# Kernel tuning notes

Hardware: AMD Instinct MI355X
Metric: run time of the kernel (lower is better)

## Reference

```python
import jax, jax.numpy as jnp
import numpy as np

N = 262144          # batch size
C = 100             # num_classes
R0, R1 = 0.95, 1.0  # recall_range
LAM = 0.5           # lambda_pauc
LS = 0.1            # label_smoothing
MAX_PAUC = R1 - R0


def setup_inputs() -> dict:
    key = jax.random.key(0)
    k1, k2 = jax.random.split(key)
    predictions = jax.random.normal(k1, (N, C), dtype=jnp.float32)
    targets = jax.random.randint(k2, (N,), 0, C)
    weight = jnp.ones((C,), dtype=jnp.float32)
    return {"predictions": predictions, "targets": targets, "weight": weight}


def _roc_curves(scores, labels):
    """Vectorized per-class ROC. scores, labels: [C, N].
    Replaces the O(N^2) per-threshold loop with sort + cumsum (tie-correct:
    tp at threshold s_j counts ALL samples with score >= s_j)."""
    order = jnp.argsort(-scores, axis=1)                      # descending
    ss = jnp.take_along_axis(scores, order, axis=1)           # [C, N]
    sl = jnp.take_along_axis(labels, order, axis=1)           # [C, N]
    cpos = jnp.cumsum(sl, axis=1)                             # cumulative positives
    # last index within each tie-group of equal scores
    neg = -ss  # ascending
    idx = jax.vmap(lambda a: jnp.searchsorted(a, a, side='right'))(neg) - 1
    tp = jnp.take_along_axis(cpos, idx, axis=1)
    cnt = (idx + 1).astype(scores.dtype)
    fp = cnt - tp
    P = cpos[:, -1:]                       # total positives per class
    Nn = scores.shape[1] - P               # total negatives per class
    tpr = jnp.where(P > 0, tp / jnp.maximum(P, 1.0), 0.0)
    fpr = jnp.where(Nn > 0, fp / jnp.maximum(Nn, 1.0), 0.0)
    return fpr, tpr


def reference(predictions, targets, weight):
    probs = jax.nn.softmax(predictions, axis=1)               # [N, C]
    onehot = jnp.eye(C, dtype=predictions.dtype)[targets]     # [N, C]
    onehot_s = (1.0 - LS) * onehot + LS / C

    # per-class binary labels (smoothed true-class value > 0.5)
    labels = (onehot_s > 0.5).astype(predictions.dtype).T     # [C, N]
    scores = probs.T                                          # [C, N]

    fpr, tpr = _roc_curves(scores, labels)
    mask = (tpr >= R0) & (tpr <= R1)
    y = jnp.maximum(tpr - R0, 0.0)
    # tpr is monotone non-decreasing, so the recall mask is contiguous and
    # trapz over the masked subset == sum over adjacent pairs both in mask.
    pm = (mask[:, :-1] & mask[:, 1:]).astype(predictions.dtype)
    pauc = jnp.sum(0.5 * (y[:, :-1] + y[:, 1:]) * (fpr[:, 1:] - fpr[:, :-1]) * pm, axis=1)  # [C]

    avg_p_auc = jnp.sum(pauc * weight) / (jnp.sum(weight) * MAX_PAUC)
    # torch computes TP/FP via .item(): the pAUC path carries no gradient
    avg_p_auc = jax.lax.stop_gradient(jnp.clip(avg_p_auc, 0.0, 1.0))

    log_probs = jax.nn.log_softmax(predictions, axis=1)
    ce_loss = -jnp.mean(jnp.sum(onehot_s * log_probs * weight, axis=1))
    pauc_loss = 1.0 - avg_p_auc ** 2
    return (1.0 - LAM) * ce_loss + LAM * pauc_loss
```

## Files before the change

### kernel.cpp

```cpp
#include <hip/hip_runtime.h>
#include <math.h>

#define WAVE 64
constexpr int   CC      = 100;
constexpr int   MAXM    = 160;
constexpr int   BUCKET  = 4096;
constexpr int   USTRIDE = 161;
constexpr int   LCAP    = 4096;
constexpr float LSMOOTH = 0.1f;
constexpr int   TILE    = 64;

__global__ __launch_bounds__(256) void k1_tile(
    const float* __restrict__ pred, const int* __restrict__ targets,
    const float* __restrict__ weight, float* __restrict__ L_out,
    float* __restrict__ pos_out, float* __restrict__ ce_partial, int N)
{
    __shared__ float tile[TILE * CC];
    __shared__ int   ttgt[TILE];
    __shared__ float tL[TILE], tpos[TILE];
    __shared__ float cered[4];
    const int tid = threadIdx.x;
    const int r0  = blockIdx.x * TILE;

    const float4* src = (const float4*)(pred + (size_t)r0 * CC);
    #pragma unroll
    for (int t = tid; t < TILE * (CC / 4); t += 256)
        *((float4*)&tile[t * 4]) = src[t];
    if (tid < TILE) ttgt[tid] = targets[r0 + tid];
    __syncthreads();

    const int x = tid & 15;
    const int G = tid >> 4;
    float w[7];
    #pragma unroll
    for (int j = 0; j < 7; ++j) {
        int c = x + 16 * j;
        w[j] = (c < CC) ? weight[c] : 0.0f;
    }
    float Wl = 0.0f;
    #pragma unroll
    for (int j = 0; j < 7; ++j) Wl += w[j];
    #pragma unroll
    for (int off = 1; off < 16; off <<= 1) Wl += __shfl_xor(Wl, off, 16);

    float ce_acc = 0.0f;
    #pragma unroll
    for (int rr = 0; rr < 4; ++rr) {
        const int r = G * 4 + rr;
        const float* rp = tile + r * CC;
        float v[7];
        #pragma unroll
        for (int j = 0; j < 7; ++j) {
            int c = x + 16 * j;
            v[j] = (c < CC) ? rp[c] : -INFINITY;
        }
        float vmax = v[0];
        #pragma unroll
        for (int j = 1; j < 7; ++j) vmax = fmaxf(vmax, v[j]);
        #pragma unroll
        for (int off = 1; off < 16; off <<= 1) vmax = fmaxf(vmax, __shfl_xor(vmax, off, 16));
        float z = 0.0f, ws = 0.0f;
        #pragma unroll
        for (int j = 0; j < 7; ++j) {
            int c = x + 16 * j;
            if (c < CC) { z += __expf(v[j] - vmax); ws += w[j] * v[j]; }
        }
        #pragma unroll
        for (int off = 1; off < 16; off <<= 1) {
            z  += __shfl_xor(z,  off, 16);
            ws += __shfl_xor(ws, off, 16);
        }
        float L = vmax + __logf(z);
        if (x == 0) {
            int t = ttgt[r];
            float pt = rp[t];
            tL[r] = L; tpos[r] = pt - L;
            ce_acc += -((1.0f - LSMOOTH) * weight[t] * (pt - L)
                        + (LSMOOTH / CC) * (ws - Wl * L));
        }
    }
    #pragma unroll
    for (int off = 32; off; off >>= 1) ce_acc += __shfl_xor(ce_acc, off, WAVE);
    if ((tid & 63) == 0) cered[tid >> 6] = ce_acc;
    __syncthreads();
    if (tid < TILE) {
        L_out[r0 + tid]   = tL[tid];
        pos_out[r0 + tid] = tpos[tid];
    }
    if (tid == 0)
        ce_partial[blockIdx.x] = cered[0] + cered[1] + cered[2] + cered[3];
}

__global__ __launch_bounds__(256) void k1b_scatter(
    const int* __restrict__ targets, const float* __restrict__ pos,
    int* __restrict__ cls_cnt, float* __restrict__ bucket, int N)
{
    __shared__ int hist[CC];
    __shared__ int base[CC];
    __shared__ int loc[CC];
    const int tid = threadIdx.x;
    const int rowsPerBlock = N / gridDim.x;
    const int r0 = blockIdx.x * rowsPerBlock;
    const int r1 = r0 + rowsPerBlock;
    for (int c = tid; c < CC; c += blockDim.x) { hist[c] = 0; loc[c] = 0; }
    __syncthreads();
    for (int r = r0 + tid; r < r1; r += blockDim.x)
        atomicAdd(&hist[targets[r]], 1);
    __syncthreads();
    for (int c = tid; c < CC; c += blockDim.x)
        base[c] = (hist[c] > 0) ? atomicAdd(&cls_cnt[c], hist[c]) : 0;
    __syncthreads();
    for (int r = r0 + tid; r < r1; r += blockDim.x) {
        int c = targets[r];
        int idx = base[c] + atomicAdd(&loc[c], 1);
        if (idx < BUCKET) bucket[(size_t)c * BUCKET + idx] = pos[r];
    }
}

__global__ __launch_bounds__(256) void k2_select(
    const float* __restrict__ bucket, const int* __restrict__ cls_cnt,
    float* __restrict__ u, int* __restrict__ m_arr, int* __restrict__ P_arr,
    float* __restrict__ wm_arr)
{
    __shared__ unsigned int keys[BUCKET];
    __shared__ unsigned int hist[256];
    __shared__ unsigned int scan[256];
    __shared__ unsigned int sel[256];
    __shared__ unsigned int s_prefix;
    __shared__ int s_rank;
    __shared__ int cnt_lt;
    const int c   = blockIdx.x;
    const int tid = threadIdx.x;
    const int P = min(cls_cnt[c], BUCKET);
    double Kd = 0.95 * (double)P;
    int kf = (int)floor(Kd);
    int m = P - kf;
    if (m > MAXM) m = MAXM;
    if (m < 0) m = 0;
    if (tid == 0) {
        m_arr[c] = m; P_arr[c] = P;
        wm_arr[c] = (float)((double)(kf + 1) - Kd);
        s_prefix = 0; s_rank = m - 1; cnt_lt = 0;
    }
    for (int i = tid; i < P; i += 256) {
        unsigned int b = __float_as_uint(bucket[(size_t)c * BUCKET + i]);
        keys[i] = (b & 0x80000000u) ? ~b : (b | 0x80000000u);
    }
    __syncthreads();
    if (m == 0) return;

    for (int shift = 24; shift >= 0; shift -= 8) {
        hist[tid] = 0;
        __syncthreads();
        unsigned int pref = s_prefix;
        for (int i = tid; i < P; i += 256) {
            unsigned int k = keys[i];
            bool match = (shift == 24) || ((k >> (shift + 8)) == pref);
            if (match) atomicAdd(&hist[(k >> shift) & 255u], 1u);
        }
        __syncthreads();
        scan[tid] = hist[tid];
        __syncthreads();
        for (int off = 1; off < 256; off <<= 1) {
            unsigned int add = (tid >= off) ? scan[tid - off] : 0u;
            __syncthreads();
            scan[tid] += add;
            __syncthreads();
        }
        int r = s_rank;
        unsigned int inc = scan[tid];
        unsigned int exc = inc - hist[tid];
        __syncthreads();
        if ((unsigned int)r >= exc && (unsigned int)r < inc) {
            s_rank   = r - (int)exc;
            s_prefix = (pref << 8) | (unsigned int)tid;
        }
        __syncthreads();
    }
    const unsigned int kth = s_prefix;

    for (int i = tid; i < P; i += 256) {
        unsigned int k = keys[i];
        if (k < kth) {
            int pslot = atomicAdd(&cnt_lt, 1);
            sel[pslot] = k;
        }
    }
    __syncthreads();
    const int nlt = cnt_lt;
    for (int j = nlt + tid; j < 256; j += 256) sel[j] = (j < m) ? kth : 0xFFFFFFFFu;
    __syncthreads();
    for (int kk = 2; kk <= 256; kk <<= 1) {
        for (int j = kk >> 1; j > 0; j >>= 1) {
            int i = tid, ixj = tid ^ j;
            if (ixj > i) {
                unsigned int a = sel[i], b = sel[ixj];
                bool up = ((i & kk) == 0);
                if ((a > b) == up) { sel[i] = b; sel[ixj] = a; }
            }
            __syncthreads();
        }
    }
    if (tid < m) {
        unsigned int k = sel[tid];
        unsigned int b = (k & 0x80000000u) ? (k & 0x7fffffffu) : ~k;
        u[c * MAXM + tid] = __uint_as_float(b);
    }
}

__device__ __forceinline__ int ubound(const float* uc, int m, float key, int maxidx) {
    int l = 0;
    #pragma unroll
    for (int s = 128; s; s >>= 1) {
        int p = l + s - 1;
        float val = uc[p < maxidx ? p : maxidx];
        l += ((p < m) && (val <= key)) ? s : 0;
    }
    return l;
}

__global__ __launch_bounds__(256) void k3a_stream(
    const float4* __restrict__ pred4, const float* __restrict__ L,
    const float* __restrict__ u, const int* __restrict__ m_arr,
    uint2* __restrict__ list, int* __restrict__ list_cnt, int list_cap,
    int* __restrict__ g_cnt, int* __restrict__ g_sum, int total4)
{
    __shared__ float umax_s[CC];
    __shared__ uint2 buf[LCAP];
    __shared__ int lcnt;
    __shared__ int gbase;
    const int tid = threadIdx.x;
    if (tid < CC) {
        int m = m_arr[tid];
        umax_s[tid] = (m > 0) ? u[tid * MAXM + m - 1] : -INFINITY;
    }
    if (tid == 0) lcnt = 0;
    __syncthreads();

    const int stride = gridDim.x * blockDim.x;
    int i = blockIdx.x * blockDim.x + tid;
    int j = i % 25;
    int n = i / 25;
    const int dj = stride % 25, dn = stride / 25;
    while (i < total4) {
        float4 v = pred4[i];
        float Ln = L[n];
        float4 um = *((const float4*)&umax_s[j * 4]);
        float s0 = v.x - Ln, s1 = v.y - Ln, s2 = v.z - Ln, s3 = v.w - Ln;
        #pragma unroll
        for (int q = 0; q < 4; ++q) {
            float sc = (q == 0) ? s0 : (q == 1) ? s1 : (q == 2) ? s2 : s3;
            float mx = (q == 0) ? um.x : (q == 1) ? um.y : (q == 2) ? um.z : um.w;
            if (sc < mx) {
                int c = j * 4 + q;
                int idx = atomicAdd(&lcnt, 1);
                if (idx < LCAP) {
                    buf[idx] = make_uint2((unsigned int)c, __float_as_uint(sc));
                } else {
                    int m = m_arr[c];
                    int l = ubound(u + c * MAXM, m, sc, MAXM - 1);
                    atomicAdd(&g_cnt[c], 1);
                    atomicAdd(&g_sum[c], m - 1 - l);
                }
            }
        }
        i += stride; j += dj; n += dn;
        if (j >= 25) { j -= 25; n += 1; }
    }
    __syncthreads();
    int cnt = min(lcnt, LCAP);
    if (tid == 0) gbase = atomicAdd(list_cnt, cnt);
    __syncthreads();
    const int base0 = gbase;
    for (int k = tid; k < cnt; k += 256) {
        int gi = base0 + k;
        if (gi < list_cap) {
            list[gi] = buf[k];
        } else {
            uint2 e = buf[k];
            int c = (int)e.x; float sc = __uint_as_float(e.y);
            int m = m_arr[c];
            int l = ubound(u + c * MAXM, m, sc, MAXM - 1);
            atomicAdd(&g_cnt[c], 1);
            atomicAdd(&g_sum[c], m - 1 - l);
        }
    }
}

__global__ __launch_bounds__(256) void k3b_rank(
    const uint2* __restrict__ list, const int* __restrict__ list_cnt, int list_cap,
    const float* __restrict__ u, const int* __restrict__ m_arr,
    int* __restrict__ g_cnt, int* __restrict__ g_sum)
{
    __shared__ float us[CC * USTRIDE];
    __shared__ int sm[CC];
    __shared__ int lcnt[CC], lsum[CC];
    const int tid = threadIdx.x;
    for (int c = tid; c < CC; c += 256) { sm[c] = m_arr[c]; lcnt[c] = 0; lsum[c] = 0; }
    for (int t = tid; t < CC * MAXM; t += 256) {
        int c = t / MAXM, k = t - c * MAXM;
        us[c * USTRIDE + k] = u[t];
    }
    __syncthreads();
    const int n = min(*list_cnt, list_cap);
    const int stride = gridDim.x * blockDim.x;
    for (int idx = blockIdx.x * blockDim.x + tid; idx < n; idx += stride) {
        uint2 e = list[idx];
        int c = (int)e.x;
        float key = __uint_as_float(e.y);
        int m = sm[c];
        int l = ubound(us + c * USTRIDE, m, key, USTRIDE - 1);
        atomicAdd(&lcnt[c], 1);
        atomicAdd(&lsum[c], m - 1 - l);
    }
    __syncthreads();
    for (int c = tid; c < CC; c += 256) {
        if (lcnt[c]) { atomicAdd(&g_cnt[c], lcnt[c]); atomicAdd(&g_sum[c], lsum[c]); }
    }
}

__global__ __launch_bounds__(256) void k4_final(
    const float* __restrict__ ce_partial, int nPartial,
    const float* __restrict__ weight, const int* __restrict__ P_arr,
    const int* __restrict__ m_arr, const float* __restrict__ wm_arr,
    const int* __restrict__ g_cnt, const int* __restrict__ g_sum,
    float* __restrict__ out, int N)
{
    __shared__ double r1[256], r2[256], r3[256];
    double ce = 0.0;
    for (int i = threadIdx.x; i < nPartial; i += blockDim.x) ce += (double)ce_partial[i];
    double p = 0.0, wsum = 0.0;
    for (int c = threadIdx.x; c < CC; c += blockDim.x) {
        int P = P_arr[c], m = m_arr[c];
        double wgt = (double)weight[c];
        long long Nn = (long long)N - P;
        if (P > 0 && Nn > 0 && m > 0) {
            double wm = (double)wm_arr[c];
            double S   = (double)g_sum[c] + wm * (double)g_cnt[c];
            double sub = 0.5 * (double)(m - 1) * (double)(m - 2) + wm * (double)(m - 1);
            double pc  = (S - sub) / ((double)Nn * (double)P);
            if (pc < 0.0) pc = 0.0;
            p += pc * wgt;
        }
        wsum += wgt;
    }
    r1[threadIdx.x] = ce; r2[threadIdx.x] = p; r3[threadIdx.x] = wsum;
    __syncthreads();
    for (int off = blockDim.x >> 1; off; off >>= 1) {
        if ((int)threadIdx.x < off) {
            r1[threadIdx.x] += r1[threadIdx.x + off];
            r2[threadIdx.x] += r2[threadIdx.x + off];
            r3[threadIdx.x] += r3[threadIdx.x + off];
        }
        __syncthreads();
    }
    if (threadIdx.x == 0) {
        double ce_loss = r1[0] / (double)N;
        double avg = r2[0] / (r3[0] * 0.05);
        avg = fmin(fmax(avg, 0.0), 1.0);
        out[0] = (float)(0.5 * ce_loss + 0.5 * (1.0 - avg * avg));
    }
}

extern "C" void kernel_launch(void* const* d_in, const int* in_sizes, int n_in,
                              void* d_out, int out_size, void* d_ws, size_t ws_size,
                              hipStream_t stream) {
    (void)n_in; (void)out_size;
    const float* pred    = (const float*)d_in[0];
    const int*   targets = (const int*)d_in[1];
    const float* weight  = (const float*)d_in[2];
    float* out = (float*)d_out;
    const int N = in_sizes[1];

    const int K1_BLOCKS = N / TILE;
    char* base = (char*)d_ws;
    size_t off = 0;
    auto take = [&](size_t bytes) { char* q = base + off; off += (bytes + 15) & ~(size_t)15; return q; };
    float* L_ws       = (float*)take((size_t)N * 4);
    float* pos_ws     = (float*)take((size_t)N * 4);
    float* ce_partial = (float*)take((size_t)K1_BLOCKS * 4);
    float* u          = (float*)take((size_t)CC * MAXM * 4);
    int*   m_arr      = (int*)take(CC * 4);
    int*   P_arr      = (int*)take(CC * 4);
    float* wm_arr     = (float*)take(CC * 4);
    int*   zero_blk   = (int*)take(304 * 4);
    int*   cls_cnt  = zero_blk;
    int*   g_cnt    = zero_blk + CC;
    int*   g_sum    = zero_blk + 2 * CC;
    int*   list_cnt = zero_blk + 3 * CC;
    float* bucket     = (float*)take((size_t)CC * BUCKET * 4);
    uint2* list       = (uint2*)(base + off);
    long long rem     = (long long)ws_size - (long long)off;
    int list_cap      = (rem > 0) ? (int)(rem / 8) : 0;

    hipMemsetAsync(zero_blk, 0, 304 * 4, stream);

    k1_tile<<<K1_BLOCKS, 256, 0, stream>>>(pred, targets, weight, L_ws, pos_ws,
                                           ce_partial, N);
    k1b_scatter<<<256, 256, 0, stream>>>(targets, pos_ws, cls_cnt, bucket, N);
    k2_select<<<CC, 256, 0, stream>>>(bucket, cls_cnt, u, m_arr, P_arr, wm_arr);
    const int total4 = (int)((size_t)N * CC / 4);
    k3a_stream<<<1024, 256, 0, stream>>>((const float4*)pred, L_ws, u, m_arr,
                                         list, list_cnt, list_cap, g_cnt, g_sum, total4);
    k3b_rank<<<512, 256, 0, stream>>>(list, list_cnt, list_cap, u, m_arr, g_cnt, g_sum);
    k4_final<<<1, 256, 0, stream>>>(ce_partial, K1_BLOCKS, weight, P_arr, m_arr, wm_arr,
                                    g_cnt, g_sum, out, N);
}
```

Before: 261.9 us.

## Fuse stream, rank and final reduction into one kernel with last-block finish

Merges the candidate-streaming, ranking and final-reduction kernels into a single kernel. Each block ranks its own shared-memory candidate buffer against u in global memory and aggregates per-class counts locally. The last block to finish, detected with an atomic counter, computes the final loss. The hipMemset is replaced by zeroing inside k1. This removes three launches, the global list round-trip and the memset, at the cost of ranking against u from global/L2 instead of an LDS copy.

```diff
diff --git a/kernel.cpp b/kernel.cpp
--- a/kernel.cpp
+++ b/kernel.cpp
@@ -5,15 +5,16 @@
 constexpr int   CC      = 100;
 constexpr int   MAXM    = 160;
 constexpr int   BUCKET  = 4096;
-constexpr int   USTRIDE = 161;
 constexpr int   LCAP    = 4096;
 constexpr float LSMOOTH = 0.1f;
 constexpr int   TILE    = 64;
+constexpr int   ZN      = 3 * CC + 8;
 
 __global__ __launch_bounds__(256) void k1_tile(
     const float* __restrict__ pred, const int* __restrict__ targets,
     const float* __restrict__ weight, float* __restrict__ L_out,
-    float* __restrict__ pos_out, float* __restrict__ ce_partial, int N)
+    float* __restrict__ pos_out, float* __restrict__ ce_partial,
+    int* __restrict__ zero_blk, int N)
 {
     __shared__ float tile[TILE * CC];
     __shared__ int   ttgt[TILE];
@@ -21,6 +22,9 @@
     __shared__ float cered[4];
     const int tid = threadIdx.x;
     const int r0  = blockIdx.x * TILE;
+
+    if (blockIdx.x == 0)
+        for (int i = tid; i < ZN; i += 256) zero_blk[i] = 0;
 
     const float4* src = (const float4*)(pred + (size_t)r0 * CC);
     #pragma unroll
@@ -219,22 +223,30 @@
     return l;
 }
 
-__global__ __launch_bounds__(256) void k3a_stream(
+__global__ __launch_bounds__(256) void k3_fused(
     const float4* __restrict__ pred4, const float* __restrict__ L,
     const float* __restrict__ u, const int* __restrict__ m_arr,
-    uint2* __restrict__ list, int* __restrict__ list_cnt, int list_cap,
-    int* __restrict__ g_cnt, int* __restrict__ g_sum, int total4)
+    int* __restrict__ g_cnt, int* __restrict__ g_sum, int* __restrict__ done,
+    const float* __restrict__ ce_partial, int nPartial,
+    const float* __restrict__ weight, const int* __restrict__ P_arr,
+    const float* __restrict__ wm_arr, float* __restrict__ out,
+    int N, int total4)
 {
     __shared__ float umax_s[CC];
+    __shared__ int   sm[CC];
+    __shared__ int   lcnt[CC], lsum[CC];
     __shared__ uint2 buf[LCAP];
-    __shared__ int lcnt;
-    __shared__ int gbase;
+    __shared__ int   lc;
+    __shared__ int   isLast;
+    __shared__ double r1[256], r2[256], r3[256];
     const int tid = threadIdx.x;
     if (tid < CC) {
         int m = m_arr[tid];
+        sm[tid] = m;
         umax_s[tid] = (m > 0) ? u[tid * MAXM + m - 1] : -INFINITY;
-    }
-    if (tid == 0) lcnt = 0;
+        lcnt[tid] = 0; lsum[tid] = 0;
+    }
+    if (tid == 0) lc = 0;
     __syncthreads();
 
     const int stride = gridDim.x * blockDim.x;
@@ -253,14 +265,14 @@
             float mx = (q == 0) ? um.x : (q == 1) ? um.y : (q == 2) ? um.z : um.w;
             if (sc < mx) {
                 int c = j * 4 + q;
-                int idx = atomicAdd(&lcnt, 1);
+                int idx = atomicAdd(&lc, 1);
                 if (idx < LCAP) {
                     buf[idx] = make_uint2((unsigned int)c, __float_as_uint(sc));
                 } else {
-                    int m = m_arr[c];
+                    int m = sm[c];
                     int l = ubound(u + c * MAXM, m, sc, MAXM - 1);
-                    atomicAdd(&g_cnt[c], 1);
-                    atomicAdd(&g_sum[c], m - 1 - l);
+                    atomicAdd(&lcnt[c], 1);
+                    atomicAdd(&lsum[c], m - 1 - l);
                 }
             }
         }
@@ -268,48 +280,14 @@
         if (j >= 25) { j -= 25; n += 1; }
     }
     __syncthreads();
-    int cnt = min(lcnt, LCAP);
-    if (tid == 0) gbase = atomicAdd(list_cnt, cnt);
-    __syncthreads();
-    const int base0 = gbase;
+
+    const int cnt = min(lc, LCAP);
     for (int k = tid; k < cnt; k += 256) {
-        int gi = base0 + k;
-        if (gi < list_cap) {
-            list[gi] = buf[k];
-        } else {
-            uint2 e = buf[k];
-            int c = (int)e.x; float sc = __uint_as_float(e.y);
-            int m = m_arr[c];
-            int l = ubound(u + c * MAXM, m, sc, MAXM - 1);
-            atomicAdd(&g_cnt[c], 1);
-            atomicAdd(&g_sum[c], m - 1 - l);
-        }
-    }
-}
-
-__global__ __launch_bounds__(256) void k3b_rank(
-    const uint2* __restrict__ list, const int* __restrict__ list_cnt, int list_cap,
-    const float* __restrict__ u, const int* __restrict__ m_arr,
-    int* __restrict__ g_cnt, int* __restrict__ g_sum)
-{
-    __shared__ float us[CC * USTRIDE];
-    __shared__ int sm[CC];
-    __shared__ int lcnt[CC], lsum[CC];
-    const int tid = threadIdx.x;
-    for (int c = tid; c < CC; c += 256) { sm[c] = m_arr[c]; lcnt[c] = 0; lsum[c] = 0; }
-    for (int t = tid; t < CC * MAXM; t += 256) {
-        int c = t / MAXM, k = t - c * MAXM;
-        us[c * USTRIDE + k] = u[t];
-    }
-    __syncthreads();
-    const int n = min(*list_cnt, list_cap);
-    const int stride = gridDim.x * blockDim.x;
-    for (int idx = blockIdx.x * blockDim.x + tid; idx < n; idx += stride) {
-        uint2 e = list[idx];
+        uint2 e = buf[k];
         int c = (int)e.x;
         float key = __uint_as_float(e.y);
         int m = sm[c];
-        int l = ubound(us + c * USTRIDE, m, key, USTRIDE - 1);
+        int l = ubound(u + c * MAXM, m, key, MAXM - 1);
         atomicAdd(&lcnt[c], 1);
         atomicAdd(&lsum[c], m - 1 - l);
     }
@@ -317,26 +295,27 @@
     for (int c = tid; c < CC; c += 256) {
         if (lcnt[c]) { atomicAdd(&g_cnt[c], lcnt[c]); atomicAdd(&g_sum[c], lsum[c]); }
     }
-}
-
-__global__ __launch_bounds__(256) void k4_final(
-    const float* __restrict__ ce_partial, int nPartial,
-    const float* __restrict__ weight, const int* __restrict__ P_arr,
-    const int* __restrict__ m_arr, const float* __restrict__ wm_arr,
-    const int* __restrict__ g_cnt, const int* __restrict__ g_sum,
-    float* __restrict__ out, int N)
-{
-    __shared__ double r1[256], r2[256], r3[256];
+
+    if (tid == 0) {
+        __threadfence();
+        int t = atomicAdd(done, 1);
+        isLast = (t == (int)gridDim.x - 1);
+    }
+    __syncthreads();
+    if (!isLast) return;
+    __threadfence();
+
     double ce = 0.0;
-    for (int i = threadIdx.x; i < nPartial; i += blockDim.x) ce += (double)ce_partial[i];
+    for (int k = tid; k < nPartial; k += 256) ce += (double)ce_partial[k];
     double p = 0.0, wsum = 0.0;
-    for (int c = threadIdx.x; c < CC; c += blockDim.x) {
-        int P = P_arr[c], m = m_arr[c];
+    for (int c = tid; c < CC; c += 256) {
+        int P = P_arr[c], m = sm[c];
         double wgt = (double)weight[c];
         long long Nn = (long long)N - P;
         if (P > 0 && Nn > 0 && m > 0) {
             double wm = (double)wm_arr[c];
-            double S   = (double)g_sum[c] + wm * (double)g_cnt[c];
+            double S   = (double)atomicAdd(&g_sum[c], 0)
+                       + wm * (double)atomicAdd(&g_cnt[c], 0);
             double sub = 0.5 * (double)(m - 1) * (double)(m - 2) + wm * (double)(m - 1);
             double pc  = (S - sub) / ((double)Nn * (double)P);
             if (pc < 0.0) pc = 0.0;
@@ -344,17 +323,17 @@
         }
         wsum += wgt;
     }
-    r1[threadIdx.x] = ce; r2[threadIdx.x] = p; r3[threadIdx.x] = wsum;
-    __syncthreads();
-    for (int off = blockDim.x >> 1; off; off >>= 1) {
-        if ((int)threadIdx.x < off) {
-            r1[threadIdx.x] += r1[threadIdx.x + off];
-            r2[threadIdx.x] += r2[threadIdx.x + off];
-            r3[threadIdx.x] += r3[threadIdx.x + off];
-        }
-        __syncthreads();
-    }
-    if (threadIdx.x == 0) {
+    r1[tid] = ce; r2[tid] = p; r3[tid] = wsum;
+    __syncthreads();
+    for (int off = 128; off; off >>= 1) {
+        if (tid < off) {
+            r1[tid] += r1[tid + off];
+            r2[tid] += r2[tid + off];
+            r3[tid] += r3[tid + off];
+        }
+        __syncthreads();
+    }
+    if (tid == 0) {
         double ce_loss = r1[0] / (double)N;
         double avg = r2[0] / (r3[0] * 0.05);
         avg = fmin(fmax(avg, 0.0), 1.0);
@@ -365,7 +344,7 @@
 extern "C" void kernel_launch(void* const* d_in, const int* in_sizes, int n_in,
                               void* d_out, int out_size, void* d_ws, size_t ws_size,
                               hipStream_t stream) {
-    (void)n_in; (void)out_size;
+    (void)n_in; (void)out_size; (void)ws_size;
     const float* pred    = (const float*)d_in[0];
     const int*   targets = (const int*)d_in[1];
     const float* weight  = (const float*)d_in[2];
@@ -383,26 +362,19 @@
     int*   m_arr      = (int*)take(CC * 4);
     int*   P_arr      = (int*)take(CC * 4);
     float* wm_arr     = (float*)take(CC * 4);
-    int*   zero_blk   = (int*)take(304 * 4);
+    int*   zero_blk   = (int*)take(ZN * 4);
     int*   cls_cnt  = zero_blk;
     int*   g_cnt    = zero_blk + CC;
     int*   g_sum    = zero_blk + 2 * CC;
-    int*   list_cnt = zero_blk + 3 * CC;
+    int*   done     = zero_blk + 3 * CC;
     float* bucket     = (float*)take((size_t)CC * BUCKET * 4);
-    uint2* list       = (uint2*)(base + off);
-    long long rem     = (long long)ws_size - (long long)off;
-    int list_cap      = (rem > 0) ? (int)(rem / 8) : 0;
-
-    hipMemsetAsync(zero_blk, 0, 304 * 4, stream);
 
     k1_tile<<<K1_BLOCKS, 256, 0, stream>>>(pred, targets, weight, L_ws, pos_ws,
-                                           ce_partial, N);
+                                           ce_partial, zero_blk, N);
     k1b_scatter<<<256, 256, 0, stream>>>(targets, pos_ws, cls_cnt, bucket, N);
     k2_select<<<CC, 256, 0, stream>>>(bucket, cls_cnt, u, m_arr, P_arr, wm_arr);
     const int total4 = (int)((size_t)N * CC / 4);
-    k3a_stream<<<1024, 256, 0, stream>>>((const float4*)pred, L_ws, u, m_arr,
-                                         list, list_cnt, list_cap, g_cnt, g_sum, total4);
-    k3b_rank<<<512, 256, 0, stream>>>(list, list_cnt, list_cap, u, m_arr, g_cnt, g_sum);
-    k4_final<<<1, 256, 0, stream>>>(ce_partial, K1_BLOCKS, weight, P_arr, m_arr, wm_arr,
-                                    g_cnt, g_sum, out, N);
-}
+    k3_fused<<<1024, 256, 0, stream>>>((const float4*)pred, L_ws, u, m_arr,
+                                       g_cnt, g_sum, done, ce_partial, K1_BLOCKS,
+                                       weight, P_arr, wm_arr, out, N, total4);
+}
```

New measurement: 265.5 us. About the same (+1.4%).
